# Kernel tuning notes

Measured on AMD Instinct MI355X. Metric: run time of the kernel, lower is better.

## Reference

```python
import jax, jax.numpy as jnp
import numpy as np

B, T_IN, F_IN = 2048, 128, 64
H = 256
OUT_LEN = 32
FC_HID = 256


def _gru_cell(x, h, W_ih, W_hh, b_ih, b_hh):
    # torch.nn.GRUCell semantics. W_ih: (3H, in), W_hh: (3H, H)
    gi = x @ W_ih.T + b_ih
    gh = h @ W_hh.T + b_hh
    i_r, i_z, i_n = jnp.split(gi, 3, axis=-1)
    h_r, h_z, h_n = jnp.split(gh, 3, axis=-1)
    r = jax.nn.sigmoid(i_r + h_r)
    z = jax.nn.sigmoid(i_z + h_z)
    n = jnp.tanh(i_n + r * h_n)
    return (1.0 - z) * n + z * h


def setup_inputs() -> dict:
    key = jax.random.key(0)
    ks = jax.random.split(key, 16)
    s = 0.05
    return {
        "x": jax.random.normal(ks[0], (B, T_IN, F_IN), jnp.float32),
        "h": jax.random.normal(ks[1], (B, H), jnp.float32),
        "enc_Wih": jax.random.normal(ks[2], (3 * H, F_IN), jnp.float32) * s,
        "enc_Whh": jax.random.normal(ks[3], (3 * H, H), jnp.float32) * s,
        "enc_bih": jnp.zeros((3 * H,), jnp.float32),
        "enc_bhh": jnp.zeros((3 * H,), jnp.float32),
        "dec_Wih": jax.random.normal(ks[4], (3 * H, 1), jnp.float32) * s,
        "dec_Whh": jax.random.normal(ks[5], (3 * H, H), jnp.float32) * s,
        "dec_bih": jnp.zeros((3 * H,), jnp.float32),
        "dec_bhh": jnp.zeros((3 * H,), jnp.float32),
        "attn_Wq": jax.random.normal(ks[6], (1, H), jnp.float32) * s,
        "attn_bq": jnp.zeros((H,), jnp.float32),
        "fc1_W": jax.random.normal(ks[7], (FC_HID, H), jnp.float32) * (2.0 / H) ** 0.5,
        "fc1_b": jnp.zeros((FC_HID,), jnp.float32),
        "fc2_W": jax.random.normal(ks[8], (1, FC_HID), jnp.float32) * (2.0 / FC_HID) ** 0.5,
        "fc2_b": jnp.zeros((1,), jnp.float32),
    }


def reference(x, h, enc_Wih, enc_Whh, enc_bih, enc_bhh,
              dec_Wih, dec_Whh, dec_bih, dec_bhh,
              attn_Wq, attn_bq, fc1_W, fc1_b, fc2_W, fc2_b):
    scale = 1.0 / jnp.sqrt(jnp.float32(H))

    # --- encoder: GRU over T_IN steps, keep all hidden states ---
    def enc_step(hc, xt):
        hn = _gru_cell(xt, hc, enc_Wih, enc_Whh, enc_bih, enc_bhh)
        return hn, hn

    _, hs = jax.lax.scan(enc_step, h, jnp.swapaxes(x, 0, 1))  # (T, B, H)
    hs = jnp.swapaxes(hs, 0, 1)  # (B, T, H)

    def dec_step(prev, _):
        q = prev @ attn_Wq + attn_bq                    # (B, H)
        scores = jnp.einsum('bh,bth->bt', q, hs) * scale
        w = jax.nn.softmax(scores, axis=-1)
        ctx = jnp.einsum('bt,bth->bh', w, hs)           # attention embedding
        hd = _gru_cell(prev, ctx, dec_Wih, dec_Whh, dec_bih, dec_bhh)
        out = jnp.maximum(hd @ fc1_W.T + fc1_b, 0.0) @ fc2_W.T + fc2_b  # (B,1)
        return out, out

    prev0 = x[:, -1, 0:1]
    _, outs = jax.lax.scan(dec_step, prev0, None, length=OUT_LEN)  # (S, B, 1)
    return jnp.swapaxes(outs[..., 0], 0, 1)  # (B, S)
```

## Files before the change

### kernel.cpp

```cpp
#include <hip/hip_runtime.h>
#include <hip/hip_bf16.h>


#define B_    2048
#define T_    128
#define F_    64
#define H_    256
#define OUT_  32
#define BT_   16
#define NTH_  512
#define NB_   (B_ / BT_)
#define PD_   6
#define HSTR_ 264
#define FSTR_ 260
#define XSTR_ 72
#define SSTR_ 260

#define PK_EHH_ 0
#define PK_EIH_ (PK_EHH_ + 3 * H_ * H_)
#define PK_DHH_ (PK_EIH_ + 3 * H_ * F_)
#define PK_F1_  (PK_DHH_ + 3 * H_ * H_)
#define W_TOT_  (PK_F1_ + H_ * H_)

typedef __attribute__((ext_vector_type(8))) short bf16x8;
typedef __attribute__((ext_vector_type(4))) float f32x4;

__device__ __forceinline__ f32x4 mfma16(bf16x8 a, bf16x8 b, f32x4 c) {
  return __builtin_amdgcn_mfma_f32_16x16x32_bf16(a, b, c, 0, 0, 0);
}
__device__ __forceinline__ float sigm_(float x) { return 1.0f / (1.0f + __expf(-x)); }
__device__ __forceinline__ float tanh_(float x) {
  x = fminf(15.0f, fmaxf(-15.0f, x));
  float e = __expf(2.0f * x);
  return (e - 1.0f) / (e + 1.0f);
}

__global__ __launch_bounds__(256) void af_convert_weights(
    const float* __restrict__ eWih, const float* __restrict__ eWhh,
    const float* __restrict__ dWhh, const float* __restrict__ f1W,
    __hip_bfloat16* __restrict__ wb) {
  for (int i = blockIdx.x * blockDim.x + threadIdx.x; i < W_TOT_;
       i += gridDim.x * blockDim.x) {
    float v;
    int o, chunk, r, ln, e, q, ck, c, kk, row, col;
    if (i < PK_EIH_) {
      o = i;
      chunk = o >> 9; r = o & 511; ln = r >> 3; e = r & 7;
      q = chunk % 3; ck = chunk / 3; c = ck >> 3; kk = ck & 7;
      row = q * H_ + c * 16 + (ln & 15);
      col = kk * 32 + (ln >> 4) * 8 + e;
      v = eWhh[row * H_ + col];
    } else if (i < PK_DHH_) {
      o = i - PK_EIH_;
      chunk = o >> 9; r = o & 511; ln = r >> 3; e = r & 7;
      q = chunk % 3; ck = chunk / 3; c = ck >> 1; kk = ck & 1;
      row = q * H_ + c * 16 + (ln & 15);
      col = kk * 32 + (ln >> 4) * 8 + e;
      v = eWih[row * F_ + col];
    } else if (i < PK_F1_) {
      o = i - PK_DHH_;
      chunk = o >> 9; r = o & 511; ln = r >> 3; e = r & 7;
      q = chunk % 3; ck = chunk / 3; c = ck >> 3; kk = ck & 7;
      row = q * H_ + c * 16 + (ln & 15);
      col = kk * 32 + (ln >> 4) * 8 + e;
      v = dWhh[row * H_ + col];
    } else {
      o = i - PK_F1_;
      chunk = o >> 9; r = o & 511; ln = r >> 3; e = r & 7;
      c = chunk >> 3; kk = chunk & 7;
      row = c * 16 + (ln & 15);
      col = kk * 32 + (ln >> 4) * 8 + e;
      v = f1W[row * H_ + col];
    }
    wb[i] = __float2bfloat16(v);
  }
}

__global__ __launch_bounds__(NTH_, 2) void af_fused_kernel(
    const float* __restrict__ x,
    const float* __restrict__ h0,
    const float* __restrict__ ebih,
    const float* __restrict__ ebhh,
    const float* __restrict__ dWih,
    const float* __restrict__ dbih,
    const float* __restrict__ dbhh,
    const float* __restrict__ aWq,
    const float* __restrict__ abq,
    const float* __restrict__ f1b,
    const float* __restrict__ f2W,
    const float* __restrict__ f2b,
    const __hip_bfloat16* __restrict__ eWihB,
    const __hip_bfloat16* __restrict__ eWhhB,
    const __hip_bfloat16* __restrict__ dWhhB,
    const __hip_bfloat16* __restrict__ f1WB,
    __hip_bfloat16* __restrict__ hs,
    float* __restrict__ dout)
{
  __shared__ __hip_bfloat16 sh_h[2][BT_ * HSTR_];
  __shared__ __hip_bfloat16 sh_l[2][BT_ * HSTR_];
  __shared__ float          s_hf[2][BT_ * FSTR_];
  __shared__ __hip_bfloat16 sh_x[2][BT_ * XSTR_];
  __shared__ __hip_bfloat16 sh_xl[2][BT_ * XSTR_];
  __shared__ float s_A[BT_ * T_], s_C[BT_ * T_];
  __shared__ float s_ebr[H_], s_ebz[H_], s_ebin[H_], s_ebhn[H_];
  __shared__ float s_dbr[H_], s_dbz[H_], s_dbin[H_], s_dbhn[H_];
  __shared__ float s_dwih[3 * H_];
  __shared__ float s_wq[H_], s_bq[H_], s_f1b[H_], s_f2w[H_];
  __shared__ float s_f2b;
  __shared__ float s_prev[BT_];
  __shared__ float s_scr[BT_ * SSTR_];

  const int tid  = threadIdx.x;
  const int b0   = blockIdx.x * BT_;
  const int lane = tid & 63;
  const int wid  = tid >> 6;
  const int quad = lane >> 4;
  const int l16  = lane & 15;
  const int mg   = tid >> 5;
  const int cg   = tid & 31;
  const int lofs = lane * 8;

  bf16x8 ah[8], al[8], ax[2], axl[2];
  bf16x8 rb[PD_], rz[PD_], rn[PD_];

  auto load_enc = [&](int j) {
    const int slot = j % PD_;
    const int s2 = j < 10 ? 0 : 1;
    const int lo = j - s2 * 10;
    const int c = 2 * wid + s2;
    const __hip_bfloat16* p;
    if (lo < 8) p = eWhhB + (size_t)((c * 8 + lo) * 3) * 512 + lofs;
    else        p = eWihB + (size_t)((c * 2 + (lo - 8)) * 3) * 512 + lofs;
    rb[slot] = *(const bf16x8*)p;
    rz[slot] = *(const bf16x8*)(p + 512);
    rn[slot] = *(const bf16x8*)(p + 1024);
  };
  auto load_dec = [&](int j) {
    const int slot = j % PD_;
    const __hip_bfloat16* p =
        dWhhB + (size_t)(((2 * wid + (j >> 3)) * 8 + (j & 7)) * 3) * 512 + lofs;
    rb[slot] = *(const bf16x8*)p;
    rz[slot] = *(const bf16x8*)(p + 512);
    rn[slot] = *(const bf16x8*)(p + 1024);
  };
  auto load_fc = [&](int j) {
    const int slot = j % PD_;
    rb[slot] = *(const bf16x8*)(
        f1WB + (size_t)((2 * wid + (j >> 3)) * 8 + (j & 7)) * 512 + lofs);
  };
  auto use_whh = [&](int kk, int slot, f32x4& ar, f32x4& az, f32x4& anh) {
    ar  = mfma16(al[kk], rb[slot], ar);  ar  = mfma16(ah[kk], rb[slot], ar);
    az  = mfma16(al[kk], rz[slot], az);  az  = mfma16(ah[kk], rz[slot], az);
    anh = mfma16(al[kk], rn[slot], anh); anh = mfma16(ah[kk], rn[slot], anh);
  };
  auto use_wih = [&](int kk, int slot, f32x4& ar, f32x4& az, f32x4& ani) {
    ar  = mfma16(axl[kk], rb[slot], ar);  ar  = mfma16(ax[kk], rb[slot], ar);
    az  = mfma16(axl[kk], rz[slot], az);  az  = mfma16(ax[kk], rz[slot], az);
    ani = mfma16(axl[kk], rn[slot], ani); ani = mfma16(ax[kk], rn[slot], ani);
  };
  auto use_fc = [&](int kk, int slot, f32x4& a1) {
    a1 = mfma16(al[kk], rb[slot], a1);
    a1 = mfma16(ah[kk], rb[slot], a1);
  };

  for (int g = tid; g < H_; g += NTH_) {
    s_ebr[g]  = ebih[g]          + ebhh[g];
    s_ebz[g]  = ebih[H_ + g]     + ebhh[H_ + g];
    s_ebin[g] = ebih[2 * H_ + g];
    s_ebhn[g] = ebhh[2 * H_ + g];
    s_dbr[g]  = dbih[g]          + dbhh[g];
    s_dbz[g]  = dbih[H_ + g]     + dbhh[H_ + g];
    s_dbin[g] = dbih[2 * H_ + g];
    s_dbhn[g] = dbhh[2 * H_ + g];
    s_wq[g]   = aWq[g];
    s_bq[g]   = abq[g];
    s_f1b[g]  = f1b[g];
    s_f2w[g]  = f2W[g];
  }
  for (int g = tid; g < 3 * H_; g += NTH_) s_dwih[g] = dWih[g];
  if (tid == 0) s_f2b = f2b[0];

  {
    const float* hp = h0 + (size_t)(b0 + mg) * H_ + cg * 8;
    float4 v0 = *(const float4*)(hp);
    float4 v1 = *(const float4*)(hp + 4);
    float vv[8] = {v0.x, v0.y, v0.z, v0.w, v1.x, v1.y, v1.z, v1.w};
#pragma unroll
    for (int j = 0; j < 8; ++j) {
      float v = vv[j];
      s_hf[0][mg * FSTR_ + cg * 8 + j] = v;
      __hip_bfloat16 hi = __float2bfloat16(v);
      sh_h[0][mg * HSTR_ + cg * 8 + j] = hi;
      sh_l[0][mg * HSTR_ + cg * 8 + j] = __float2bfloat16(v - __bfloat162float(hi));
    }
    float2 xv = *(const float2*)(x + ((size_t)(b0 + mg) * T_) * F_ + cg * 2);
    __hip_bfloat16 xh0 = __float2bfloat16(xv.x);
    __hip_bfloat16 xh1 = __float2bfloat16(xv.y);
    sh_x[0][mg * XSTR_ + cg * 2]      = xh0;
    sh_x[0][mg * XSTR_ + cg * 2 + 1]  = xh1;
    sh_xl[0][mg * XSTR_ + cg * 2]     = __float2bfloat16(xv.x - __bfloat162float(xh0));
    sh_xl[0][mg * XSTR_ + cg * 2 + 1] = __float2bfloat16(xv.y - __bfloat162float(xh1));
  }
#pragma unroll
  for (int j = 0; j < PD_; ++j) load_enc(j);
  __syncthreads();

  int cur = 0;
  for (int t = 0; t < T_; ++t) {
    const int nxt = cur ^ 1;

    float2 xv;
    if (t + 1 < T_)
      xv = *(const float2*)(x + ((size_t)(b0 + mg) * T_ + (t + 1)) * F_ + cg * 2);
    if (t > 0) {
      uint4 hv = *(const uint4*)&sh_h[cur][mg * HSTR_ + cg * 8];
      *(uint4*)&hs[((size_t)(b0 + mg) * T_ + (t - 1)) * H_ + cg * 8] = hv;
    }

#pragma unroll
    for (int kk = 0; kk < 8; ++kk) {
      ah[kk] = *(const bf16x8*)&sh_h[cur][l16 * HSTR_ + kk * 32 + quad * 8];
      al[kk] = *(const bf16x8*)&sh_l[cur][l16 * HSTR_ + kk * 32 + quad * 8];
    }
#pragma unroll
    for (int kk = 0; kk < 2; ++kk) {
      ax[kk]  = *(const bf16x8*)&sh_x[cur][l16 * XSTR_ + kk * 32 + quad * 8];
      axl[kk] = *(const bf16x8*)&sh_xl[cur][l16 * XSTR_ + kk * 32 + quad * 8];
    }

    f32x4 z4 = {0.f, 0.f, 0.f, 0.f};
    f32x4 ar0 = z4, az0 = z4, ani0 = z4, anh0 = z4;
    f32x4 ar1 = z4, az1 = z4, ani1 = z4, anh1 = z4;

#pragma unroll
    for (int j = 0; j < 20; ++j) {
      if (j < 8)       use_whh(j,      j % PD_, ar0, az0, anh0);
      else if (j < 10) use_wih(j - 8,  j % PD_, ar0, az0, ani0);
      else if (j < 18) use_whh(j - 10, j % PD_, ar1, az1, anh1);
      else             use_wih(j - 18, j % PD_, ar1, az1, ani1);
      if (j + PD_ < 20) load_enc(j + PD_);

      if (j == 9 || j == 19) {
        const int s2 = (j == 9) ? 0 : 1;
        const f32x4& ar = (j == 9) ? ar0 : ar1;
        const f32x4& az = (j == 9) ? az0 : az1;
        const f32x4& ani = (j == 9) ? ani0 : ani1;
        const f32x4& anh = (j == 9) ? anh0 : anh1;
        const int g = 16 * (2 * wid + s2) + l16;
        const float br_ = s_ebr[g], bz_ = s_ebz[g], bin_ = s_ebin[g], bhn_ = s_ebhn[g];
#pragma unroll
        for (int i = 0; i < 4; ++i) {
          const int m = quad * 4 + i;
          float r = sigm_(ar[i] + br_);
          float z = sigm_(az[i] + bz_);
          float n = tanh_(ani[i] + bin_ + r * (anh[i] + bhn_));
          float hold = s_hf[cur][m * FSTR_ + g];
          float hn = (1.0f - z) * n + z * hold;
          s_hf[nxt][m * FSTR_ + g] = hn;
          __hip_bfloat16 hi = __float2bfloat16(hn);
          sh_h[nxt][m * HSTR_ + g] = hi;
          sh_l[nxt][m * HSTR_ + g] = __float2bfloat16(hn - __bfloat162float(hi));
        }
      }
    }

    if (t > 0) {
      const float* hp = &s_hf[cur][mg * FSTR_ + cg * 8];
      float pa = 0.f, pc = 0.f;
#pragma unroll
      for (int j = 0; j < 8; ++j) {
        float hvf = hp[j];
        pa += hvf * s_wq[cg * 8 + j];
        pc += hvf * s_bq[cg * 8 + j];
      }
#pragma unroll
      for (int off = 16; off >= 1; off >>= 1) {
        pa += __shfl_xor(pa, off, 64);
        pc += __shfl_xor(pc, off, 64);
      }
      if (cg == 0) {
        s_A[mg * T_ + (t - 1)] = pa;
        s_C[mg * T_ + (t - 1)] = pc;
      }
    }
    if (t + 1 < T_) {
      __hip_bfloat16 xh0 = __float2bfloat16(xv.x);
      __hip_bfloat16 xh1 = __float2bfloat16(xv.y);
      sh_x[nxt][mg * XSTR_ + cg * 2]      = xh0;
      sh_x[nxt][mg * XSTR_ + cg * 2 + 1]  = xh1;
      sh_xl[nxt][mg * XSTR_ + cg * 2]     = __float2bfloat16(xv.x - __bfloat162float(xh0));
      sh_xl[nxt][mg * XSTR_ + cg * 2 + 1] = __float2bfloat16(xv.y - __bfloat162float(xh1));
#pragma unroll
      for (int j = 0; j < PD_; ++j) load_enc(j);
    }
    __syncthreads();
    cur = nxt;
  }

  {
    uint4 hv = *(const uint4*)&sh_h[cur][mg * HSTR_ + cg * 8];
    *(uint4*)&hs[((size_t)(b0 + mg) * T_ + (T_ - 1)) * H_ + cg * 8] = hv;
    const float* hp = &s_hf[cur][mg * FSTR_ + cg * 8];
    float pa = 0.f, pc = 0.f;
#pragma unroll
    for (int j = 0; j < 8; ++j) {
      float hvf = hp[j];
      pa += hvf * s_wq[cg * 8 + j];
      pc += hvf * s_bq[cg * 8 + j];
    }
#pragma unroll
    for (int off = 16; off >= 1; off >>= 1) {
      pa += __shfl_xor(pa, off, 64);
      pc += __shfl_xor(pc, off, 64);
    }
    if (cg == 0) {
      s_A[mg * T_ + (T_ - 1)] = pa;
      s_C[mg * T_ + (T_ - 1)] = pc;
    }
  }

  float prevr = x[((size_t)(b0 + mg) * T_ + (T_ - 1)) * F_];
  if (tid < BT_)
    s_prev[tid] = x[((size_t)(b0 + tid) * T_ + (T_ - 1)) * F_];
  __syncthreads();

  for (int s = 0; s < OUT_; ++s) {
    {
      float4 a4 = *(const float4*)(s_A + mg * T_ + cg * 4);
      float4 c4 = *(const float4*)(s_C + mg * T_ + cg * 4);
      const float pv = prevr;
      float sc0 = (pv * a4.x + c4.x) * 0.0625f;
      float sc1 = (pv * a4.y + c4.y) * 0.0625f;
      float sc2 = (pv * a4.z + c4.z) * 0.0625f;
      float sc3 = (pv * a4.w + c4.w) * 0.0625f;
      float mx = fmaxf(fmaxf(sc0, sc1), fmaxf(sc2, sc3));
#pragma unroll
      for (int off = 16; off >= 1; off >>= 1) mx = fmaxf(mx, __shfl_xor(mx, off, 64));
      float e0 = __expf(sc0 - mx), e1 = __expf(sc1 - mx);
      float e2 = __expf(sc2 - mx), e3 = __expf(sc3 - mx);
      float ss = e0 + e1 + e2 + e3;
#pragma unroll
      for (int off = 16; off >= 1; off >>= 1) ss += __shfl_xor(ss, off, 64);
      const float inv = 1.0f / ss;
      float4 wv = make_float4(e0 * inv, e1 * inv, e2 * inv, e3 * inv);
      *(float4*)&s_scr[mg * SSTR_ + cg * 4] = wv;
    }

    {
#pragma unroll
      for (int j = 0; j < PD_; ++j) load_dec(j);

      float acc[8] = {0.f, 0.f, 0.f, 0.f, 0.f, 0.f, 0.f, 0.f};
      const __hip_bfloat16* hp = hs + (size_t)(b0 + mg) * T_ * H_ + cg * 8;
      const float* wp = &s_scr[mg * SSTR_];
      uint4 bA[8], bB[8];
#pragma unroll
      for (int u = 0; u < 8; ++u) bA[u] = *(const uint4*)(hp + (size_t)u * H_);
      auto p2fma = [&](const uint4& hv, float wt) {
        acc[0] = fmaf(wt, __uint_as_float(hv.x << 16),         acc[0]);
        acc[1] = fmaf(wt, __uint_as_float(hv.x & 0xFFFF0000u), acc[1]);
        acc[2] = fmaf(wt, __uint_as_float(hv.y << 16),         acc[2]);
        acc[3] = fmaf(wt, __uint_as_float(hv.y & 0xFFFF0000u), acc[3]);
        acc[4] = fmaf(wt, __uint_as_float(hv.z << 16),         acc[4]);
        acc[5] = fmaf(wt, __uint_as_float(hv.z & 0xFFFF0000u), acc[5]);
        acc[6] = fmaf(wt, __uint_as_float(hv.w << 16),         acc[6]);
        acc[7] = fmaf(wt, __uint_as_float(hv.w & 0xFFFF0000u), acc[7]);
      };
      for (int tb = 0; tb < T_; tb += 16) {
#pragma unroll
        for (int u = 0; u < 8; ++u) bB[u] = *(const uint4*)(hp + (size_t)(tb + 8 + u) * H_);
#pragma unroll
        for (int u = 0; u < 8; ++u) p2fma(bA[u], wp[tb + u]);
        if (tb + 16 < T_) {
#pragma unroll
          for (int u = 0; u < 8; ++u) bA[u] = *(const uint4*)(hp + (size_t)(tb + 16 + u) * H_);
        }
#pragma unroll
        for (int u = 0; u < 8; ++u) p2fma(bB[u], wp[tb + 8 + u]);
      }
#pragma unroll
      for (int j = 0; j < 8; ++j) {
        float v = acc[j];
        s_hf[0][mg * FSTR_ + cg * 8 + j] = v;
        __hip_bfloat16 hi = __float2bfloat16(v);
        sh_h[0][mg * HSTR_ + cg * 8 + j] = hi;
        sh_l[0][mg * HSTR_ + cg * 8 + j] = __float2bfloat16(v - __bfloat162float(hi));
      }
    }
    __syncthreads();

    {
#pragma unroll
      for (int kk = 0; kk < 8; ++kk) {
        ah[kk] = *(const bf16x8*)&sh_h[0][l16 * HSTR_ + kk * 32 + quad * 8];
        al[kk] = *(const bf16x8*)&sh_l[0][l16 * HSTR_ + kk * 32 + quad * 8];
      }
      f32x4 z4 = {0.f, 0.f, 0.f, 0.f};
      f32x4 ar0 = z4, az0 = z4, anh0 = z4;
      f32x4 ar1 = z4, az1 = z4, anh1 = z4;
#pragma unroll
      for (int j = 0; j < 16; ++j) {
        if (j < 8) use_whh(j,     j % PD_, ar0, az0, anh0);
        else       use_whh(j - 8, j % PD_, ar1, az1, anh1);
        if (j + PD_ < 16) load_dec(j + PD_);

        if (j == 7 || j == 15) {
          const int s2 = (j == 7) ? 0 : 1;
          const f32x4& ar = (j == 7) ? ar0 : ar1;
          const f32x4& az = (j == 7) ? az0 : az1;
          const f32x4& anh = (j == 7) ? anh0 : anh1;
          const int g = 16 * (2 * wid + s2) + l16;
          const float dr = s_dbr[g], dz = s_dbz[g], din = s_dbin[g], dhn = s_dbhn[g];
          const float wir = s_dwih[g], wiz = s_dwih[H_ + g], win = s_dwih[2 * H_ + g];
#pragma unroll
          for (int i = 0; i < 4; ++i) {
            const int m = quad * 4 + i;
            const float pv = s_prev[m];
            float r = sigm_(ar[i] + pv * wir + dr);
            float z = sigm_(az[i] + pv * wiz + dz);
            float n = tanh_(pv * win + din + r * (anh[i] + dhn));
            float ctxv = s_hf[0][m * FSTR_ + g];
            float hd = (1.0f - z) * n + z * ctxv;
            __hip_bfloat16 hi = __float2bfloat16(hd);
            sh_h[1][m * HSTR_ + g] = hi;
            sh_l[1][m * HSTR_ + g] = __float2bfloat16(hd - __bfloat162float(hi));
          }
        }
      }
    }
    __syncthreads();

    {
#pragma unroll
      for (int kk = 0; kk < 8; ++kk) {
        ah[kk] = *(const bf16x8*)&sh_h[1][l16 * HSTR_ + kk * 32 + quad * 8];
        al[kk] = *(const bf16x8*)&sh_l[1][l16 * HSTR_ + kk * 32 + quad * 8];
      }
#pragma unroll
      for (int j = 0; j < PD_; ++j) load_fc(j);
      f32x4 z4 = {0.f, 0.f, 0.f, 0.f};
      f32x4 a10 = z4, a11 = z4;
#pragma unroll
      for (int j = 0; j < 16; ++j) {
        if (j < 8) use_fc(j,     j % PD_, a10);
        else       use_fc(j - 8, j % PD_, a11);
        if (j + PD_ < 16) load_fc(j + PD_);

        if (j == 7 || j == 15) {
          const int s2 = (j == 7) ? 0 : 1;
          const f32x4& a1 = (j == 7) ? a10 : a11;
          const int jcol = 16 * (2 * wid + s2) + l16;
          const float bj = s_f1b[jcol];
#pragma unroll
          for (int i = 0; i < 4; ++i) {
            const int m = quad * 4 + i;
            s_scr[m * SSTR_ + jcol] = fmaxf(a1[i] + bj, 0.0f);
          }
        }
      }
    }
    __syncthreads();

    {
      const float* ap = &s_scr[mg * SSTR_ + cg * 8];
      float p = 0.f;
#pragma unroll
      for (int j = 0; j < 8; ++j)
        p += ap[j] * s_f2w[cg * 8 + j];
#pragma unroll
      for (int off = 16; off >= 1; off >>= 1) p += __shfl_xor(p, off, 64);
      float o = p + s_f2b;
      prevr = o;
      if (cg == 0) {
        s_prev[mg] = o;
        dout[(size_t)(b0 + mg) * OUT_ + s] = o;
      }
    }
  }
}

extern "C" void kernel_launch(void* const* d_in, const int* in_sizes, int n_in,
                              void* d_out, int out_size, void* d_ws, size_t ws_size,
                              hipStream_t stream) {
  (void)in_sizes; (void)n_in; (void)out_size; (void)ws_size;
  const float* x    = (const float*)d_in[0];
  const float* h0   = (const float*)d_in[1];
  const float* eWih = (const float*)d_in[2];
  const float* eWhh = (const float*)d_in[3];
  const float* ebih = (const float*)d_in[4];
  const float* ebhh = (const float*)d_in[5];
  const float* dWih = (const float*)d_in[6];
  const float* dWhh = (const float*)d_in[7];
  const float* dbih = (const float*)d_in[8];
  const float* dbhh = (const float*)d_in[9];
  const float* aWq  = (const float*)d_in[10];
  const float* abq  = (const float*)d_in[11];
  const float* f1W  = (const float*)d_in[12];
  const float* f1b  = (const float*)d_in[13];
  const float* f2W  = (const float*)d_in[14];
  const float* f2b  = (const float*)d_in[15];

  __hip_bfloat16* hs = (__hip_bfloat16*)d_ws;
  __hip_bfloat16* wb = (__hip_bfloat16*)((char*)d_ws + (size_t)B_ * T_ * H_ * 2);

  hipLaunchKernelGGL(af_convert_weights, dim3(256), dim3(256), 0, stream,
                     eWih, eWhh, dWhh, f1W, wb);
  hipLaunchKernelGGL(af_fused_kernel, dim3(NB_), dim3(NTH_), 0, stream,
                     x, h0, ebih, ebhh, dWih, dbih, dbhh, aWq, abq, f1b, f2W, f2b,
                     wb + PK_EIH_, wb + PK_EHH_, wb + PK_DHH_, wb + PK_F1_,
                     hs, (float*)d_out);
}
```

Baseline: 1.942 ms.

## Deepen weight prefetch pipeline and keep global loads in flight across barriers

Raises the register prefetch depth for streamed weight fragments from 6 to 8 slots. It replaces __syncthreads with a barrier that waits only on LDS counters, so outstanding global weight loads can stay in flight across the barrier. It also moves the decoder and FC weight preloads earlier, before barriers and alongside the attention context loads, and adds sched_barriers to pin the load/MFMA interleaving. The cost is more VGPR pressure, which may cause spills or lower occupancy. There is also a risk that the hand-placed barriers limit compiler scheduling.

```diff
diff --git a/kernel.cpp b/kernel.cpp
--- a/kernel.cpp
+++ b/kernel.cpp
@@ -10,7 +10,7 @@
 #define BT_   16
 #define NTH_  512
 #define NB_   (B_ / BT_)
-#define PD_   6
+#define PD_   8
 #define HSTR_ 264
 #define FSTR_ 260
 #define XSTR_ 72
@@ -33,6 +33,12 @@
   x = fminf(15.0f, fmaxf(-15.0f, x));
   float e = __expf(2.0f * x);
   return (e - 1.0f) / (e + 1.0f);
+}
+__device__ __forceinline__ void barrier_lds() {
+  __builtin_amdgcn_sched_barrier(0);
+  asm volatile("s_waitcnt lgkmcnt(0)" ::: "memory");
+  __builtin_amdgcn_s_barrier();
+  __builtin_amdgcn_sched_barrier(0);
 }
 
 __global__ __launch_bounds__(256) void af_convert_weights(
@@ -124,7 +130,7 @@
   bf16x8 rb[PD_], rz[PD_], rn[PD_];
 
   auto load_enc = [&](int j) {
-    const int slot = j % PD_;
+    const int slot = j & 7;
     const int s2 = j < 10 ? 0 : 1;
     const int lo = j - s2 * 10;
     const int c = 2 * wid + s2;
@@ -136,7 +142,7 @@
     rn[slot] = *(const bf16x8*)(p + 1024);
   };
   auto load_dec = [&](int j) {
-    const int slot = j % PD_;
+    const int slot = j & 7;
     const __hip_bfloat16* p =
         dWhhB + (size_t)(((2 * wid + (j >> 3)) * 8 + (j & 7)) * 3) * 512 + lofs;
     rb[slot] = *(const bf16x8*)p;
@@ -144,7 +150,7 @@
     rn[slot] = *(const bf16x8*)(p + 1024);
   };
   auto load_fc = [&](int j) {
-    const int slot = j % PD_;
+    const int slot = j & 7;
     rb[slot] = *(const bf16x8*)(
         f1WB + (size_t)((2 * wid + (j >> 3)) * 8 + (j & 7)) * 512 + lofs);
   };
@@ -203,7 +209,7 @@
   }
 #pragma unroll
   for (int j = 0; j < PD_; ++j) load_enc(j);
-  __syncthreads();
+  barrier_lds();
 
   int cur = 0;
   for (int t = 0; t < T_; ++t) {
@@ -234,10 +240,10 @@
 
 #pragma unroll
     for (int j = 0; j < 20; ++j) {
-      if (j < 8)       use_whh(j,      j % PD_, ar0, az0, anh0);
-      else if (j < 10) use_wih(j - 8,  j % PD_, ar0, az0, ani0);
-      else if (j < 18) use_whh(j - 10, j % PD_, ar1, az1, anh1);
-      else             use_wih(j - 18, j % PD_, ar1, az1, ani1);
+      if (j < 8)       use_whh(j,      j & 7, ar0, az0, anh0);
+      else if (j < 10) use_wih(j - 8,  j & 7, ar0, az0, ani0);
+      else if (j < 18) use_whh(j - 10, j & 7, ar1, az1, anh1);
+      else             use_wih(j - 18, j & 7, ar1, az1, ani1);
       if (j + PD_ < 20) load_enc(j + PD_);
 
       if (j == 9 || j == 19) {
@@ -262,6 +268,7 @@
           sh_l[nxt][m * HSTR_ + g] = __float2bfloat16(hn - __bfloat162float(hi));
         }
       }
+      __builtin_amdgcn_sched_barrier(0);
     }
 
     if (t > 0) {
@@ -293,7 +300,7 @@
 #pragma unroll
       for (int j = 0; j < PD_; ++j) load_enc(j);
     }
-    __syncthreads();
+    barrier_lds();
     cur = nxt;
   }
 
@@ -347,15 +354,15 @@
     }
 
     {
-#pragma unroll
-      for (int j = 0; j < PD_; ++j) load_dec(j);
-
       float acc[8] = {0.f, 0.f, 0.f, 0.f, 0.f, 0.f, 0.f, 0.f};
       const __hip_bfloat16* hp = hs + (size_t)(b0 + mg) * T_ * H_ + cg * 8;
       const float* wp = &s_scr[mg * SSTR_];
       uint4 bA[8], bB[8];
 #pragma unroll
       for (int u = 0; u < 8; ++u) bA[u] = *(const uint4*)(hp + (size_t)u * H_);
+#pragma unroll
+      for (int j = 0; j < PD_; ++j) load_dec(j);
+      __builtin_amdgcn_sched_barrier(0);
       auto p2fma = [&](const uint4& hv, float wt) {
         acc[0] = fmaf(wt, __uint_as_float(hv.x << 16),         acc[0]);
         acc[1] = fmaf(wt, __uint_as_float(hv.x & 0xFFFF0000u), acc[1]);
@@ -387,7 +394,7 @@
         sh_l[0][mg * HSTR_ + cg * 8 + j] = __float2bfloat16(v - __bfloat162float(hi));
       }
     }
-    __syncthreads();
+    barrier_lds();
 
     {
 #pragma unroll
@@ -400,8 +407,8 @@
       f32x4 ar1 = z4, az1 = z4, anh1 = z4;
 #pragma unroll
       for (int j = 0; j < 16; ++j) {
-        if (j < 8) use_whh(j,     j % PD_, ar0, az0, anh0);
-        else       use_whh(j - 8, j % PD_, ar1, az1, anh1);
+        if (j < 8) use_whh(j,     j & 7, ar0, az0, anh0);
+        else       use_whh(j - 8, j & 7, ar1, az1, anh1);
         if (j + PD_ < 16) load_dec(j + PD_);
 
         if (j == 7 || j == 15) {
@@ -426,9 +433,12 @@
             sh_l[1][m * HSTR_ + g] = __float2bfloat16(hd - __bfloat162float(hi));
           }
         }
-      }
-    }
-    __syncthreads();
+        __builtin_amdgcn_sched_barrier(0);
+      }
+#pragma unroll
+      for (int j = 0; j < PD_; ++j) load_fc(j);
+    }
+    barrier_lds();
 
     {
 #pragma unroll
@@ -436,14 +446,12 @@
         ah[kk] = *(const bf16x8*)&sh_h[1][l16 * HSTR_ + kk * 32 + quad * 8];
         al[kk] = *(const bf16x8*)&sh_l[1][l16 * HSTR_ + kk * 32 + quad * 8];
       }
-#pragma unroll
-      for (int j = 0; j < PD_; ++j) load_fc(j);
       f32x4 z4 = {0.f, 0.f, 0.f, 0.f};
       f32x4 a10 = z4, a11 = z4;
 #pragma unroll
       for (int j = 0; j < 16; ++j) {
-        if (j < 8) use_fc(j,     j % PD_, a10);
-        else       use_fc(j - 8, j % PD_, a11);
+        if (j < 8) use_fc(j,     j & 7, a10);
+        else       use_fc(j - 8, j & 7, a11);
         if (j + PD_ < 16) load_fc(j + PD_);
 
         if (j == 7 || j == 15) {
@@ -457,9 +465,10 @@
             s_scr[m * SSTR_ + jcol] = fmaxf(a1[i] + bj, 0.0f);
           }
         }
-      }
-    }
-    __syncthreads();
+        __builtin_amdgcn_sched_barrier(0);
+      }
+    }
+    barrier_lds();
 
     {
       const float* ap = &s_scr[mg * SSTR_ + cg * 8];
```

Measured after the change: 2.912 ms. +50.0%, slower.

## Halve batch tile to 8 rows per block and raise occupancy target

Applied to the files above, without the earlier changes.

Shrinks the per-block batch tile from 16 to 8 rows, doubling the number of blocks, and raises launch bounds to 4 blocks per SM. Thread-to-data mappings, reductions and MFMA A-operand row indexing are reworked so the 16-row MFMA tiles use duplicated rows and only half the quads write results. The hs stores and loads become nontemporal 64-bit accesses, and the fc weight prefetch is hoisted to overlap with the decoder GRU. Half of each MFMA's work is now wasted and register pressure under the tighter launch bound may cause spills, in exchange for more parallelism across the device.

```diff
diff --git a/kernel.cpp b/kernel.cpp
--- a/kernel.cpp
+++ b/kernel.cpp
@@ -7,7 +7,7 @@
 #define F_    64
 #define H_    256
 #define OUT_  32
-#define BT_   16
+#define BT_   8
 #define NTH_  512
 #define NB_   (B_ / BT_)
 #define PD_   6
@@ -24,6 +24,7 @@
 
 typedef __attribute__((ext_vector_type(8))) short bf16x8;
 typedef __attribute__((ext_vector_type(4))) float f32x4;
+typedef unsigned long long u64;
 
 __device__ __forceinline__ f32x4 mfma16(bf16x8 a, bf16x8 b, f32x4 c) {
   return __builtin_amdgcn_mfma_f32_16x16x32_bf16(a, b, c, 0, 0, 0);
@@ -76,7 +77,7 @@
   }
 }
 
-__global__ __launch_bounds__(NTH_, 2) void af_fused_kernel(
+__global__ __launch_bounds__(NTH_, 4) void af_fused_kernel(
     const float* __restrict__ x,
     const float* __restrict__ h0,
     const float* __restrict__ ebih,
@@ -116,8 +117,9 @@
   const int wid  = tid >> 6;
   const int quad = lane >> 4;
   const int l16  = lane & 15;
-  const int mg   = tid >> 5;
-  const int cg   = tid & 31;
+  const int arow = l16 & 7;
+  const int mg   = tid >> 6;
+  const int cg   = tid & 63;
   const int lofs = lane * 8;
 
   bf16x8 ah[8], al[8], ax[2], axl[2];
@@ -181,25 +183,20 @@
   if (tid == 0) s_f2b = f2b[0];
 
   {
-    const float* hp = h0 + (size_t)(b0 + mg) * H_ + cg * 8;
-    float4 v0 = *(const float4*)(hp);
-    float4 v1 = *(const float4*)(hp + 4);
-    float vv[8] = {v0.x, v0.y, v0.z, v0.w, v1.x, v1.y, v1.z, v1.w};
-#pragma unroll
-    for (int j = 0; j < 8; ++j) {
+    const float4 v0 = *(const float4*)(h0 + (size_t)(b0 + mg) * H_ + cg * 4);
+    float vv[4] = {v0.x, v0.y, v0.z, v0.w};
+#pragma unroll
+    for (int j = 0; j < 4; ++j) {
       float v = vv[j];
-      s_hf[0][mg * FSTR_ + cg * 8 + j] = v;
+      s_hf[0][mg * FSTR_ + cg * 4 + j] = v;
       __hip_bfloat16 hi = __float2bfloat16(v);
-      sh_h[0][mg * HSTR_ + cg * 8 + j] = hi;
-      sh_l[0][mg * HSTR_ + cg * 8 + j] = __float2bfloat16(v - __bfloat162float(hi));
-    }
-    float2 xv = *(const float2*)(x + ((size_t)(b0 + mg) * T_) * F_ + cg * 2);
-    __hip_bfloat16 xh0 = __float2bfloat16(xv.x);
-    __hip_bfloat16 xh1 = __float2bfloat16(xv.y);
-    sh_x[0][mg * XSTR_ + cg * 2]      = xh0;
-    sh_x[0][mg * XSTR_ + cg * 2 + 1]  = xh1;
-    sh_xl[0][mg * XSTR_ + cg * 2]     = __float2bfloat16(xv.x - __bfloat162float(xh0));
-    sh_xl[0][mg * XSTR_ + cg * 2 + 1] = __float2bfloat16(xv.y - __bfloat162float(xh1));
+      sh_h[0][mg * HSTR_ + cg * 4 + j] = hi;
+      sh_l[0][mg * HSTR_ + cg * 4 + j] = __float2bfloat16(v - __bfloat162float(hi));
+    }
+    float xv = x[((size_t)(b0 + mg) * T_) * F_ + cg];
+    __hip_bfloat16 xh = __float2bfloat16(xv);
+    sh_x[0][mg * XSTR_ + cg]  = xh;
+    sh_xl[0][mg * XSTR_ + cg] = __float2bfloat16(xv - __bfloat162float(xh));
   }
 #pragma unroll
   for (int j = 0; j < PD_; ++j) load_enc(j);
@@ -209,23 +206,24 @@
   for (int t = 0; t < T_; ++t) {
     const int nxt = cur ^ 1;
 
-    float2 xv;
+    float xv = 0.f;
     if (t + 1 < T_)
-      xv = *(const float2*)(x + ((size_t)(b0 + mg) * T_ + (t + 1)) * F_ + cg * 2);
+      xv = x[((size_t)(b0 + mg) * T_ + (t + 1)) * F_ + cg];
     if (t > 0) {
-      uint4 hv = *(const uint4*)&sh_h[cur][mg * HSTR_ + cg * 8];
-      *(uint4*)&hs[((size_t)(b0 + mg) * T_ + (t - 1)) * H_ + cg * 8] = hv;
+      u64 hv = *(const u64*)&sh_h[cur][mg * HSTR_ + cg * 4];
+      __builtin_nontemporal_store(
+          hv, (u64*)&hs[((size_t)(b0 + mg) * T_ + (t - 1)) * H_ + cg * 4]);
     }
 
 #pragma unroll
     for (int kk = 0; kk < 8; ++kk) {
-      ah[kk] = *(const bf16x8*)&sh_h[cur][l16 * HSTR_ + kk * 32 + quad * 8];
-      al[kk] = *(const bf16x8*)&sh_l[cur][l16 * HSTR_ + kk * 32 + quad * 8];
+      ah[kk] = *(const bf16x8*)&sh_h[cur][arow * HSTR_ + kk * 32 + quad * 8];
+      al[kk] = *(const bf16x8*)&sh_l[cur][arow * HSTR_ + kk * 32 + quad * 8];
     }
 #pragma unroll
     for (int kk = 0; kk < 2; ++kk) {
-      ax[kk]  = *(const bf16x8*)&sh_x[cur][l16 * XSTR_ + kk * 32 + quad * 8];
-      axl[kk] = *(const bf16x8*)&sh_xl[cur][l16 * XSTR_ + kk * 32 + quad * 8];
+      ax[kk]  = *(const bf16x8*)&sh_x[cur][arow * XSTR_ + kk * 32 + quad * 8];
+      axl[kk] = *(const bf16x8*)&sh_xl[cur][arow * XSTR_ + kk * 32 + quad * 8];
     }
 
     f32x4 z4 = {0.f, 0.f, 0.f, 0.f};
@@ -248,33 +246,35 @@
         const f32x4& anh = (j == 9) ? anh0 : anh1;
         const int g = 16 * (2 * wid + s2) + l16;
         const float br_ = s_ebr[g], bz_ = s_ebz[g], bin_ = s_ebin[g], bhn_ = s_ebhn[g];
-#pragma unroll
-        for (int i = 0; i < 4; ++i) {
-          const int m = quad * 4 + i;
-          float r = sigm_(ar[i] + br_);
-          float z = sigm_(az[i] + bz_);
-          float n = tanh_(ani[i] + bin_ + r * (anh[i] + bhn_));
-          float hold = s_hf[cur][m * FSTR_ + g];
-          float hn = (1.0f - z) * n + z * hold;
-          s_hf[nxt][m * FSTR_ + g] = hn;
-          __hip_bfloat16 hi = __float2bfloat16(hn);
-          sh_h[nxt][m * HSTR_ + g] = hi;
-          sh_l[nxt][m * HSTR_ + g] = __float2bfloat16(hn - __bfloat162float(hi));
+        if (quad < 2) {
+#pragma unroll
+          for (int i = 0; i < 4; ++i) {
+            const int m = quad * 4 + i;
+            float r = sigm_(ar[i] + br_);
+            float z = sigm_(az[i] + bz_);
+            float n = tanh_(ani[i] + bin_ + r * (anh[i] + bhn_));
+            float hold = s_hf[cur][m * FSTR_ + g];
+            float hn = (1.0f - z) * n + z * hold;
+            s_hf[nxt][m * FSTR_ + g] = hn;
+            __hip_bfloat16 hi = __float2bfloat16(hn);
+            sh_h[nxt][m * HSTR_ + g] = hi;
+            sh_l[nxt][m * HSTR_ + g] = __float2bfloat16(hn - __bfloat162float(hi));
+          }
         }
       }
     }
 
     if (t > 0) {
-      const float* hp = &s_hf[cur][mg * FSTR_ + cg * 8];
+      const float* hp = &s_hf[cur][mg * FSTR_ + cg * 4];
       float pa = 0.f, pc = 0.f;
 #pragma unroll
-      for (int j = 0; j < 8; ++j) {
+      for (int j = 0; j < 4; ++j) {
         float hvf = hp[j];
-        pa += hvf * s_wq[cg * 8 + j];
-        pc += hvf * s_bq[cg * 8 + j];
-      }
-#pragma unroll
-      for (int off = 16; off >= 1; off >>= 1) {
+        pa += hvf * s_wq[cg * 4 + j];
+        pc += hvf * s_bq[cg * 4 + j];
+      }
+#pragma unroll
+      for (int off = 32; off >= 1; off >>= 1) {
         pa += __shfl_xor(pa, off, 64);
         pc += __shfl_xor(pc, off, 64);
       }
@@ -284,12 +284,9 @@
       }
     }
     if (t + 1 < T_) {
-      __hip_bfloat16 xh0 = __float2bfloat16(xv.x);
-      __hip_bfloat16 xh1 = __float2bfloat16(xv.y);
-      sh_x[nxt][mg * XSTR_ + cg * 2]      = xh0;
-      sh_x[nxt][mg * XSTR_ + cg * 2 + 1]  = xh1;
-      sh_xl[nxt][mg * XSTR_ + cg * 2]     = __float2bfloat16(xv.x - __bfloat162float(xh0));
-      sh_xl[nxt][mg * XSTR_ + cg * 2 + 1] = __float2bfloat16(xv.y - __bfloat162float(xh1));
+      __hip_bfloat16 xh = __float2bfloat16(xv);
+      sh_x[nxt][mg * XSTR_ + cg]  = xh;
+      sh_xl[nxt][mg * XSTR_ + cg] = __float2bfloat16(xv - __bfloat162float(xh));
 #pragma unroll
       for (int j = 0; j < PD_; ++j) load_enc(j);
     }
@@ -298,18 +295,19 @@
   }
 
   {
-    uint4 hv = *(const uint4*)&sh_h[cur][mg * HSTR_ + cg * 8];
-    *(uint4*)&hs[((size_t)(b0 + mg) * T_ + (T_ - 1)) * H_ + cg * 8] = hv;
-    const float* hp = &s_hf[cur][mg * FSTR_ + cg * 8];
+    u64 hv = *(const u64*)&sh_h[cur][mg * HSTR_ + cg * 4];
+    __builtin_nontemporal_store(
+        hv, (u64*)&hs[((size_t)(b0 + mg) * T_ + (T_ - 1)) * H_ + cg * 4]);
+    const float* hp = &s_hf[cur][mg * FSTR_ + cg * 4];
     float pa = 0.f, pc = 0.f;
 #pragma unroll
-    for (int j = 0; j < 8; ++j) {
+    for (int j = 0; j < 4; ++j) {
       float hvf = hp[j];
-      pa += hvf * s_wq[cg * 8 + j];
-      pc += hvf * s_bq[cg * 8 + j];
-    }
-#pragma unroll
-    for (int off = 16; off >= 1; off >>= 1) {
+      pa += hvf * s_wq[cg * 4 + j];
+      pc += hvf * s_bq[cg * 4 + j];
+    }
+#pragma unroll
+    for (int off = 32; off >= 1; off >>= 1) {
       pa += __shfl_xor(pa, off, 64);
       pc += __shfl_xor(pc, off, 64);
     }
@@ -326,65 +324,60 @@
 
   for (int s = 0; s < OUT_; ++s) {
     {
-      float4 a4 = *(const float4*)(s_A + mg * T_ + cg * 4);
-      float4 c4 = *(const float4*)(s_C + mg * T_ + cg * 4);
+      float2 a2 = *(const float2*)(s_A + mg * T_ + cg * 2);
+      float2 c2 = *(const float2*)(s_C + mg * T_ + cg * 2);
       const float pv = prevr;
-      float sc0 = (pv * a4.x + c4.x) * 0.0625f;
-      float sc1 = (pv * a4.y + c4.y) * 0.0625f;
-      float sc2 = (pv * a4.z + c4.z) * 0.0625f;
-      float sc3 = (pv * a4.w + c4.w) * 0.0625f;
-      float mx = fmaxf(fmaxf(sc0, sc1), fmaxf(sc2, sc3));
-#pragma unroll
-      for (int off = 16; off >= 1; off >>= 1) mx = fmaxf(mx, __shfl_xor(mx, off, 64));
+      float sc0 = (pv * a2.x + c2.x) * 0.0625f;
+      float sc1 = (pv * a2.y + c2.y) * 0.0625f;
+      float mx = fmaxf(sc0, sc1);
+#pragma unroll
+      for (int off = 32; off >= 1; off >>= 1) mx = fmaxf(mx, __shfl_xor(mx, off, 64));
       float e0 = __expf(sc0 - mx), e1 = __expf(sc1 - mx);
-      float e2 = __expf(sc2 - mx), e3 = __expf(sc3 - mx);
-      float ss = e0 + e1 + e2 + e3;
-#pragma unroll
-      for (int off = 16; off >= 1; off >>= 1) ss += __shfl_xor(ss, off, 64);
+      float ss = e0 + e1;
+#pragma unroll
+      for (int off = 32; off >= 1; off >>= 1) ss += __shfl_xor(ss, off, 64);
       const float inv = 1.0f / ss;
-      float4 wv = make_float4(e0 * inv, e1 * inv, e2 * inv, e3 * inv);
-      *(float4*)&s_scr[mg * SSTR_ + cg * 4] = wv;
+      *(float2*)&s_scr[mg * SSTR_ + cg * 2] = make_float2(e0 * inv, e1 * inv);
     }
 
     {
+      float acc[4] = {0.f, 0.f, 0.f, 0.f};
+      const __hip_bfloat16* hp = hs + (size_t)(b0 + mg) * T_ * H_ + cg * 4;
+      const float* wp = &s_scr[mg * SSTR_];
+      u64 bA[8], bB[8];
+#pragma unroll
+      for (int u = 0; u < 8; ++u)
+        bA[u] = __builtin_nontemporal_load((const u64*)(hp + (size_t)u * H_));
 #pragma unroll
       for (int j = 0; j < PD_; ++j) load_dec(j);
-
-      float acc[8] = {0.f, 0.f, 0.f, 0.f, 0.f, 0.f, 0.f, 0.f};
-      const __hip_bfloat16* hp = hs + (size_t)(b0 + mg) * T_ * H_ + cg * 8;
-      const float* wp = &s_scr[mg * SSTR_];
-      uint4 bA[8], bB[8];
-#pragma unroll
-      for (int u = 0; u < 8; ++u) bA[u] = *(const uint4*)(hp + (size_t)u * H_);
-      auto p2fma = [&](const uint4& hv, float wt) {
-        acc[0] = fmaf(wt, __uint_as_float(hv.x << 16),         acc[0]);
-        acc[1] = fmaf(wt, __uint_as_float(hv.x & 0xFFFF0000u), acc[1]);
-        acc[2] = fmaf(wt, __uint_as_float(hv.y << 16),         acc[2]);
-        acc[3] = fmaf(wt, __uint_as_float(hv.y & 0xFFFF0000u), acc[3]);
-        acc[4] = fmaf(wt, __uint_as_float(hv.z << 16),         acc[4]);
-        acc[5] = fmaf(wt, __uint_as_float(hv.z & 0xFFFF0000u), acc[5]);
-        acc[6] = fmaf(wt, __uint_as_float(hv.w << 16),         acc[6]);
-        acc[7] = fmaf(wt, __uint_as_float(hv.w & 0xFFFF0000u), acc[7]);
+      auto p2fma = [&](u64 hv, float wt) {
+        unsigned lo = (unsigned)hv, hi2 = (unsigned)(hv >> 32);
+        acc[0] = fmaf(wt, __uint_as_float(lo << 16),          acc[0]);
+        acc[1] = fmaf(wt, __uint_as_float(lo & 0xFFFF0000u),  acc[1]);
+        acc[2] = fmaf(wt, __uint_as_float(hi2 << 16),         acc[2]);
+        acc[3] = fmaf(wt, __uint_as_float(hi2 & 0xFFFF0000u), acc[3]);
       };
       for (int tb = 0; tb < T_; tb += 16) {
 #pragma unroll
-        for (int u = 0; u < 8; ++u) bB[u] = *(const uint4*)(hp + (size_t)(tb + 8 + u) * H_);
+        for (int u = 0; u < 8; ++u)
+          bB[u] = __builtin_nontemporal_load((const u64*)(hp + (size_t)(tb + 8 + u) * H_));
 #pragma unroll
         for (int u = 0; u < 8; ++u) p2fma(bA[u], wp[tb + u]);
         if (tb + 16 < T_) {
 #pragma unroll
-          for (int u = 0; u < 8; ++u) bA[u] = *(const uint4*)(hp + (size_t)(tb + 16 + u) * H_);
+          for (int u = 0; u < 8; ++u)
+            bA[u] = __builtin_nontemporal_load((const u64*)(hp + (size_t)(tb + 16 + u) * H_));
         }
 #pragma unroll
         for (int u = 0; u < 8; ++u) p2fma(bB[u], wp[tb + 8 + u]);
       }
 #pragma unroll
-      for (int j = 0; j < 8; ++j) {
+      for (int j = 0; j < 4; ++j) {
         float v = acc[j];
-        s_hf[0][mg * FSTR_ + cg * 8 + j] = v;
+        s_hf[0][mg * FSTR_ + cg * 4 + j] = v;
         __hip_bfloat16 hi = __float2bfloat16(v);
-        sh_h[0][mg * HSTR_ + cg * 8 + j] = hi;
-        sh_l[0][mg * HSTR_ + cg * 8 + j] = __float2bfloat16(v - __bfloat162float(hi));
+        sh_h[0][mg * HSTR_ + cg * 4 + j] = hi;
+        sh_l[0][mg * HSTR_ + cg * 4 + j] = __float2bfloat16(v - __bfloat162float(hi));
       }
     }
     __syncthreads();
@@ -392,8 +385,8 @@
     {
 #pragma unroll
       for (int kk = 0; kk < 8; ++kk) {
-        ah[kk] = *(const bf16x8*)&sh_h[0][l16 * HSTR_ + kk * 32 + quad * 8];
-        al[kk] = *(const bf16x8*)&sh_l[0][l16 * HSTR_ + kk * 32 + quad * 8];
+        ah[kk] = *(const bf16x8*)&sh_h[0][arow * HSTR_ + kk * 32 + quad * 8];
+        al[kk] = *(const bf16x8*)&sh_l[0][arow * HSTR_ + kk * 32 + quad * 8];
       }
       f32x4 z4 = {0.f, 0.f, 0.f, 0.f};
       f32x4 ar0 = z4, az0 = z4, anh0 = z4;
@@ -412,32 +405,34 @@
           const int g = 16 * (2 * wid + s2) + l16;
           const float dr = s_dbr[g], dz = s_dbz[g], din = s_dbin[g], dhn = s_dbhn[g];
           const float wir = s_dwih[g], wiz = s_dwih[H_ + g], win = s_dwih[2 * H_ + g];
-#pragma unroll
-          for (int i = 0; i < 4; ++i) {
-            const int m = quad * 4 + i;
-            const float pv = s_prev[m];
-            float r = sigm_(ar[i] + pv * wir + dr);
-            float z = sigm_(az[i] + pv * wiz + dz);
-            float n = tanh_(pv * win + din + r * (anh[i] + dhn));
-            float ctxv = s_hf[0][m * FSTR_ + g];
-            float hd = (1.0f - z) * n + z * ctxv;
-            __hip_bfloat16 hi = __float2bfloat16(hd);
-            sh_h[1][m * HSTR_ + g] = hi;
-            sh_l[1][m * HSTR_ + g] = __float2bfloat16(hd - __bfloat162float(hi));
+          if (quad < 2) {
+#pragma unroll
+            for (int i = 0; i < 4; ++i) {
+              const int m = quad * 4 + i;
+              const float pv = s_prev[m];
+              float r = sigm_(ar[i] + pv * wir + dr);
+              float z = sigm_(az[i] + pv * wiz + dz);
+              float n = tanh_(pv * win + din + r * (anh[i] + dhn));
+              float ctxv = s_hf[0][m * FSTR_ + g];
+              float hd = (1.0f - z) * n + z * ctxv;
+              __hip_bfloat16 hi = __float2bfloat16(hd);
+              sh_h[1][m * HSTR_ + g] = hi;
+              sh_l[1][m * HSTR_ + g] = __float2bfloat16(hd - __bfloat162float(hi));
+            }
           }
         }
       }
+#pragma unroll
+      for (int j = 0; j < PD_; ++j) load_fc(j);
     }
     __syncthreads();
 
     {
 #pragma unroll
       for (int kk = 0; kk < 8; ++kk) {
-        ah[kk] = *(const bf16x8*)&sh_h[1][l16 * HSTR_ + kk * 32 + quad * 8];
-        al[kk] = *(const bf16x8*)&sh_l[1][l16 * HSTR_ + kk * 32 + quad * 8];
-      }
-#pragma unroll
-      for (int j = 0; j < PD_; ++j) load_fc(j);
+        ah[kk] = *(const bf16x8*)&sh_h[1][arow * HSTR_ + kk * 32 + quad * 8];
+        al[kk] = *(const bf16x8*)&sh_l[1][arow * HSTR_ + kk * 32 + quad * 8];
+      }
       f32x4 z4 = {0.f, 0.f, 0.f, 0.f};
       f32x4 a10 = z4, a11 = z4;
 #pragma unroll
@@ -451,10 +446,12 @@
           const f32x4& a1 = (j == 7) ? a10 : a11;
           const int jcol = 16 * (2 * wid + s2) + l16;
           const float bj = s_f1b[jcol];
-#pragma unroll
-          for (int i = 0; i < 4; ++i) {
-            const int m = quad * 4 + i;
-            s_scr[m * SSTR_ + jcol] = fmaxf(a1[i] + bj, 0.0f);
+          if (quad < 2) {
+#pragma unroll
+            for (int i = 0; i < 4; ++i) {
+              const int m = quad * 4 + i;
+              s_scr[m * SSTR_ + jcol] = fmaxf(a1[i] + bj, 0.0f);
+            }
           }
         }
       }
@@ -462,13 +459,13 @@
     __syncthreads();
 
     {
-      const float* ap = &s_scr[mg * SSTR_ + cg * 8];
+      const float* ap = &s_scr[mg * SSTR_ + cg * 4];
       float p = 0.f;
 #pragma unroll
-      for (int j = 0; j < 8; ++j)
-        p += ap[j] * s_f2w[cg * 8 + j];
-#pragma unroll
-      for (int off = 16; off >= 1; off >>= 1) p += __shfl_xor(p, off, 64);
+      for (int j = 0; j < 4; ++j)
+        p += ap[j] * s_f2w[cg * 4 + j];
+#pragma unroll
+      for (int off = 32; off >= 1; off >>= 1) p += __shfl_xor(p, off, 64);
       float o = p + s_f2b;
       prevr = o;
       if (cg == 0) {
```

Result: slower. 6.527 ms (+236.1%).
